# Optimization experiments

Hardware: AMD Instinct MI355X
Metric: run time of the kernel (lower is better)

## Reference

```python
import jax, jax.numpy as jnp
import numpy as np

N_NODES = 50000
N_EDGES = 1_600_000
REL_NUM = 16
D_IN = 64
D_OUT = 64


def setup_inputs() -> dict:
    key = jax.random.key(0)
    k_h, k_w, k_n, k_s, k_d, k_r = jax.random.split(key, 6)
    h = jax.random.normal(k_h, (N_NODES, D_IN), dtype=jnp.float32)
    # xavier_uniform over (rel_num, input_dim, output_dim): fan_in=input_dim, fan_out=output_dim
    limit = float(np.sqrt(6.0 / (D_IN + D_OUT)))
    weight = jax.random.uniform(k_w, (REL_NUM, D_IN, D_OUT), dtype=jnp.float32,
                                minval=-limit, maxval=limit)
    norm = jax.random.uniform(k_n, (N_EDGES, 1), dtype=jnp.float32)
    src = jax.random.randint(k_s, (N_EDGES,), 0, N_NODES)
    dst = jax.random.randint(k_d, (N_EDGES,), 0, N_NODES)
    rel_type = jax.random.randint(k_r, (N_EDGES,), 0, REL_NUM)
    return {"h": h, "weight": weight, "norm": norm,
            "src": src, "dst": dst, "rel_type": rel_type}


def reference(h, weight, norm, src, dst, rel_type):
    # Non-input path of R_GCN_Layer:
    #   msg_e = (h[src_e] @ weight[rel_e]) * norm_e ; h'_v = relu(sum_{e->v} msg_e)
    # Instead of gathering a [E, D_in, D_out] weight tensor per edge (huge),
    # transform every node by every relation once, then gather per (src, rel).
    n_nodes = h.shape[0]
    transformed = jnp.einsum('nd,rdo->nro', h, weight)      # [N, R, D_out]
    msg = transformed[src, rel_type] * norm                  # [E, D_out]
    agg = jax.ops.segment_sum(msg, dst, num_segments=n_nodes)  # [N, D_out]
    return jax.nn.relu(agg)
```

## Files before the change

### kernel.cpp

```cpp
#include <hip/hip_runtime.h>
#include <hip/hip_bf16.h>

#define N_NODES 50000
#define N_EDGES 1600000
#define NREL    16
#define DIM     64

#define BKT_SZ  16
#define NTILE   3125
#define NSEG_AL 50049

#define CB_SH   7
#define NCB     391
#define P1_CHUNK 2048
#define P1_GRID  782

#define CB_ARENA 8704
#define EMAX    (NCB * CB_ARENA)
#define PREP_HBLK 3125

typedef __attribute__((ext_vector_type(8))) short short8;
typedef __attribute__((ext_vector_type(4))) float float4v;
typedef __attribute__((ext_vector_type(4))) unsigned short ushort4v;

template<int IS_F32>
__device__ __forceinline__ float ldx(const void* p, size_t i) {
    if (IS_F32) {
        return ((const float*)p)[i];
    } else {
        unsigned short u = ((const unsigned short*)p)[i];
        return __uint_as_float(((unsigned)u) << 16);
    }
}

__device__ __forceinline__ float bfbits2f(unsigned short u) {
    return __uint_as_float(((unsigned)u) << 16);
}

__device__ __forceinline__ unsigned short f2bfbits(float v) {
    __hip_bfloat16 b = __float2bfloat16(v);
    unsigned short us; __builtin_memcpy(&us, &b, 2);
    return us;
}

__global__ __launch_bounds__(1024) void k_detect(
    const float* __restrict__ norm_f, int* __restrict__ flag)
{
    __shared__ int sbad;
    if (threadIdx.x == 0) sbad = 0;
    __syncthreads();
    float v = norm_f[threadIdx.x];
    int bad = (v != v || fabsf(v) > 1e3f) ? 1 : 0;
    if (bad) atomicOr(&sbad, 1);
    __syncthreads();
    if (threadIdx.x == 0) *flag = sbad ? 0 : 1;
}

__global__ __launch_bounds__(256) void k_bhist_prep(
    const int* __restrict__ dst, int* __restrict__ H,
    const void* __restrict__ h_raw, const void* __restrict__ w_raw,
    unsigned short* __restrict__ hbf, unsigned short* __restrict__ Wswz,
    const int* __restrict__ flag)
{
    __shared__ int hist[NCB];
    const int blk = blockIdx.x;
    if (blk < P1_GRID) {
        for (int i = threadIdx.x; i < NCB; i += 256) hist[i] = 0;
        __syncthreads();
        const int e0 = blk * P1_CHUNK;
        for (int i = threadIdx.x; i < P1_CHUNK; i += 256) {
            int e = e0 + i;
            if (e < N_EDGES) atomicAdd(&hist[dst[e] >> CB_SH], 1);
        }
        __syncthreads();
        for (int b = threadIdx.x; b < NCB; b += 256)
            H[blk * NCB + b] = hist[b];
    } else {
        const int f = *flag;
        const int blk2 = blk - P1_GRID;
        if (blk2 < PREP_HBLK) {
            int i0 = blk2 * 1024 + threadIdx.x * 4;
            if (f) {
                float4 v = *(const float4*)((const float*)h_raw + i0);
                ushort4v o;
                o[0] = f2bfbits(v.x); o[1] = f2bfbits(v.y);
                o[2] = f2bfbits(v.z); o[3] = f2bfbits(v.w);
                *(ushort4v*)(hbf + i0) = o;
            } else {
                *(uint2*)(hbf + i0) = *(const uint2*)((const unsigned short*)h_raw + i0);
            }
        } else {
            int rel = blk2 - PREP_HBLK;
            for (int idx = threadIdx.x; idx < 4096; idx += 256) {
                int d = idx >> 6, o = idx & 63;
                float wv = f ? ((const float*)w_raw)[(size_t)((rel << 6) + d) * 64 + o]
                             : bfbits2f(((const unsigned short*)w_raw)[(size_t)((rel << 6) + d) * 64 + o]);
                int c = d >> 5, q = (d >> 3) & 3, j = d & 7;
                Wswz[(size_t)rel * 5120 + ((c << 6) + o) * 40 + q * 8 + j] = f2bfbits(wv);
            }
        }
    }
}

__global__ __launch_bounds__(256) void k_bscan1(
    const int* __restrict__ H, int* __restrict__ OT, int* __restrict__ tot)
{
    __shared__ int col[P1_GRID];
    const int b = blockIdx.x;
    for (int i = threadIdx.x; i < P1_GRID; i += 256)
        col[i] = H[i * NCB + b];
    __syncthreads();
    if (threadIdx.x < 64) {
        const int lane = threadIdx.x;
        int carry = 0;
        for (int chunk = 0; chunk < (P1_GRID + 63) / 64; ++chunk) {
            int i = chunk * 64 + lane;
            int c = (i < P1_GRID) ? col[i] : 0;
            int incl = c;
#pragma unroll
            for (int off = 1; off < 64; off <<= 1) {
                int t = __shfl_up(incl, off, 64);
                if (lane >= off) incl += t;
            }
            if (i < P1_GRID) col[i] = carry + incl - c;
            carry += __shfl(incl, 63, 64);
        }
        if (lane == 0) tot[b] = carry;
    }
    __syncthreads();
    for (int i = threadIdx.x; i < P1_GRID; i += 256)
        OT[(size_t)b * P1_GRID + i] = col[i];
}

__global__ __launch_bounds__(64) void k_bscan2(
    const int* __restrict__ tot, int* __restrict__ base)
{
    const int lane = threadIdx.x;
    int carry = 0;
    for (int chunk = 0; chunk < (NCB + 63) / 64; ++chunk) {
        int i = chunk * 64 + lane;
        int c = (i < NCB) ? tot[i] : 0;
        int incl = c;
#pragma unroll
        for (int off = 1; off < 64; off <<= 1) {
            int t = __shfl_up(incl, off, 64);
            if (lane >= off) incl += t;
        }
        if (i < NCB) base[i] = carry + incl - c;
        carry += __shfl(incl, 63, 64);
    }
    if (lane == 0) base[NCB] = carry;
}

template<int IS_F32>
__device__ __forceinline__ void p1_body(
    const int* __restrict__ src, const int* __restrict__ dst,
    const int* __restrict__ rel, const void* __restrict__ norm_raw,
    const int* __restrict__ base, const int* __restrict__ OT,
    unsigned long long* __restrict__ R, int* curs)
{
    const int blk = blockIdx.x;
    for (int b = threadIdx.x; b < NCB; b += 256)
        curs[b] = base[b] + OT[(size_t)b * P1_GRID + blk];
    __syncthreads();
    const int e0 = blk * P1_CHUNK;
    for (int i = threadIdx.x; i < P1_CHUNK; i += 256) {
        int e = e0 + i;
        if (e >= N_EDGES) continue;
        int d = dst[e];
        int pos = atomicAdd(&curs[d >> CB_SH], 1);
        unsigned short nb = f2bfbits(ldx<IS_F32>(norm_raw, e));
        unsigned long long rec =
              (unsigned long long)(d & 127)
            | ((unsigned long long)(unsigned)src[e] << 8)
            | ((unsigned long long)(unsigned)rel[e] << 24)
            | ((unsigned long long)nb << 32);
        R[pos] = rec;
    }
}

__global__ __launch_bounds__(256) void k_p1(
    const int* __restrict__ src, const int* __restrict__ dst,
    const int* __restrict__ rel, const void* __restrict__ norm_raw,
    const int* __restrict__ base, const int* __restrict__ OT,
    unsigned long long* __restrict__ R, const int* __restrict__ flag)
{
    __shared__ int curs[NCB];
    if (*flag) p1_body<1>(src, dst, rel, norm_raw, base, OT, R, curs);
    else       p1_body<0>(src, dst, rel, norm_raw, base, OT, R, curs);
}

__global__ __launch_bounds__(256) void k_fine(
    const int* __restrict__ base,
    const unsigned long long* __restrict__ R,
    unsigned* __restrict__ packed2, unsigned short* __restrict__ normS,
    int* __restrict__ segBase, int* __restrict__ segCnt)
{
    __shared__ int cnt[128], sbl[128], curs[128];
    const int tid = threadIdx.x, cb = blockIdx.x;
    if (tid < 128) { cnt[tid] = 0; curs[tid] = 0; }
    __syncthreads();
    const int c0 = base[cb], c1 = base[cb + 1];

    for (int i = c0 + tid; i < c1; i += 256) {
        unsigned long long rec = R[i];
        int bin = (int)((rec >> 24) & 15) * 8 + (int)((rec >> 4) & 7);
        atomicAdd(&cnt[bin], 1);
    }
    __syncthreads();

    if (tid == 0) {
        int g = cb * CB_ARENA;
        for (int j = 0; j < 128; ++j) {
            sbl[j] = g;
            g += (cnt[j] + 31) & ~31;
        }
    }
    __syncthreads();

    if (tid < 128) {
        int seg = ((cb * 8 + (tid & 7)) << 4) + (tid >> 3);
        segBase[seg] = sbl[tid];
        segCnt[seg]  = cnt[tid];
    }

    for (int i = c0 + tid; i < c1; i += 256) {
        unsigned long long rec = R[i];
        int bin = (int)((rec >> 24) & 15) * 8 + (int)((rec >> 4) & 7);
        int pos = sbl[bin] + atomicAdd(&curs[bin], 1);
        packed2[pos] = (unsigned)rec & 0x00FFFF0Fu;
        normS[pos]   = (unsigned short)(rec >> 32);
    }
    __syncthreads();

    for (int p = tid; p < 128 * 32; p += 256) {
        int bin = p >> 5, j = p & 31;
        int c = cnt[bin], pe = (c + 31) & ~31;
        if (j < pe - c) {
            int pos = sbl[bin] + c + j;
            packed2[pos] = 0;
            normS[pos]   = 0;
        }
    }
}

#define MFMA_BF16 __builtin_amdgcn_mfma_f32_16x16x32_bf16

__global__ __launch_bounds__(256) void k_fused2(
    const unsigned* __restrict__ packed2,
    const unsigned short* __restrict__ normS,
    const unsigned short* __restrict__ hbf,
    const unsigned short* __restrict__ Wswz,
    const int* __restrict__ segBase,
    const int* __restrict__ segCnt,
    void* __restrict__ out, const int* __restrict__ flag)
{
    __shared__ __align__(16) unsigned short sbuf[4][16 * 72];
    __shared__ float pbuf[2][64][17];
    const int tid  = threadIdx.x;
    const int lane = tid & 63, wave = tid >> 6;
    const int n15  = lane & 15, quad = lane >> 4;
    const int tin  = wave >> 1;
    const int half = wave & 1;
    const int tile = blockIdx.x * 2 + tin;
    const bool valid = (tile < NTILE);

    float4v ac0 = {0.f,0.f,0.f,0.f}, ac1 = {0.f,0.f,0.f,0.f};
    float4v ac2 = {0.f,0.f,0.f,0.f}, ac3 = {0.f,0.f,0.f,0.f};
    unsigned short* sb_ = &sbuf[wave][0];

    if (valid) {
        const int r0 = half * 8;
        for (int r = r0; r < r0 + 8; ++r) {
            const int sgb  = segBase[tile * 16 + r];
            const int scnt = segCnt[tile * 16 + r];
            if (scnt == 0) continue;
            const int nch = (scnt + 31) >> 5;

            float4v s0 = {0.f,0.f,0.f,0.f}, s1 = {0.f,0.f,0.f,0.f};
            float4v s2 = {0.f,0.f,0.f,0.f}, s3 = {0.f,0.f,0.f,0.f};

            for (int c = 0; c < nch; ++c) {
                const int e0 = sgb + (c << 5) + (quad << 3);
                const uint4 pa = *(const uint4*)(packed2 + e0);
                const uint4 pb = *(const uint4*)(packed2 + e0 + 4);
                const ushort4v na = *(const ushort4v*)(normS + e0);
                const ushort4v nb = *(const ushort4v*)(normS + e0 + 4);

                const unsigned short* h0 = hbf + (size_t)(pa.x >> 8) * 64 + n15;
                const unsigned short* h1 = hbf + (size_t)(pa.y >> 8) * 64 + n15;
                const unsigned short* h2 = hbf + (size_t)(pa.z >> 8) * 64 + n15;
                const unsigned short* h3 = hbf + (size_t)(pa.w >> 8) * 64 + n15;
                const unsigned short* h4 = hbf + (size_t)(pb.x >> 8) * 64 + n15;
                const unsigned short* h5 = hbf + (size_t)(pb.y >> 8) * 64 + n15;
                const unsigned short* h6 = hbf + (size_t)(pb.z >> 8) * 64 + n15;
                const unsigned short* h7 = hbf + (size_t)(pb.w >> 8) * 64 + n15;

                short8 av;
                av[0] = ((int)(pa.x & 15u) == n15) ? (short)na[0] : (short)0;
                av[1] = ((int)(pa.y & 15u) == n15) ? (short)na[1] : (short)0;
                av[2] = ((int)(pa.z & 15u) == n15) ? (short)na[2] : (short)0;
                av[3] = ((int)(pa.w & 15u) == n15) ? (short)na[3] : (short)0;
                av[4] = ((int)(pb.x & 15u) == n15) ? (short)nb[0] : (short)0;
                av[5] = ((int)(pb.y & 15u) == n15) ? (short)nb[1] : (short)0;
                av[6] = ((int)(pb.z & 15u) == n15) ? (short)nb[2] : (short)0;
                av[7] = ((int)(pb.w & 15u) == n15) ? (short)nb[3] : (short)0;

#define GATHER_MFMA(S, OFF) \
                { short8 bv; \
                  bv[0] = (short)h0[OFF]; bv[1] = (short)h1[OFF]; \
                  bv[2] = (short)h2[OFF]; bv[3] = (short)h3[OFF]; \
                  bv[4] = (short)h4[OFF]; bv[5] = (short)h5[OFF]; \
                  bv[6] = (short)h6[OFF]; bv[7] = (short)h7[OFF]; \
                  S = MFMA_BF16(av, bv, S, 0, 0, 0); }

                GATHER_MFMA(s0, 0)
                GATHER_MFMA(s1, 16)
                GATHER_MFMA(s2, 32)
                GATHER_MFMA(s3, 48)
#undef GATHER_MFMA
            }

#pragma unroll
            for (int i = 0; i < 4; ++i) {
                sb_[(quad * 4 + i) * 72 +  0 + n15] = f2bfbits(s0[i]);
                sb_[(quad * 4 + i) * 72 + 16 + n15] = f2bfbits(s1[i]);
                sb_[(quad * 4 + i) * 72 + 32 + n15] = f2bfbits(s2[i]);
                sb_[(quad * 4 + i) * 72 + 48 + n15] = f2bfbits(s3[i]);
            }

            const short8 a0 = *(const short8*)(sb_ + n15 * 72 + quad * 8);
            const short8 a1 = *(const short8*)(sb_ + n15 * 72 + 32 + quad * 8);

            const unsigned short* wp = Wswz + (size_t)r * 5120;
            const short8 w00 = *(const short8*)(wp + ( 0 + n15) * 40 + quad * 8);
            const short8 w01 = *(const short8*)(wp + (16 + n15) * 40 + quad * 8);
            const short8 w02 = *(const short8*)(wp + (32 + n15) * 40 + quad * 8);
            const short8 w03 = *(const short8*)(wp + (48 + n15) * 40 + quad * 8);
            const short8 w10 = *(const short8*)(wp + (64 + n15) * 40 + quad * 8);
            const short8 w11 = *(const short8*)(wp + (80 + n15) * 40 + quad * 8);
            const short8 w12 = *(const short8*)(wp + (96 + n15) * 40 + quad * 8);
            const short8 w13 = *(const short8*)(wp + (112 + n15) * 40 + quad * 8);

            ac0 = MFMA_BF16(a0, w00, ac0, 0, 0, 0);
            ac1 = MFMA_BF16(a0, w01, ac1, 0, 0, 0);
            ac2 = MFMA_BF16(a0, w02, ac2, 0, 0, 0);
            ac3 = MFMA_BF16(a0, w03, ac3, 0, 0, 0);
            ac0 = MFMA_BF16(a1, w10, ac0, 0, 0, 0);
            ac1 = MFMA_BF16(a1, w11, ac1, 0, 0, 0);
            ac2 = MFMA_BF16(a1, w12, ac2, 0, 0, 0);
            ac3 = MFMA_BF16(a1, w13, ac3, 0, 0, 0);
        }
    }

    if (half) {
#pragma unroll
        for (int i = 0; i < 4; ++i) {
            pbuf[tin][lane][i]      = ac0[i];
            pbuf[tin][lane][4 + i]  = ac1[i];
            pbuf[tin][lane][8 + i]  = ac2[i];
            pbuf[tin][lane][12 + i] = ac3[i];
        }
    }
    __syncthreads();
    if (!half && valid) {
#pragma unroll
        for (int i = 0; i < 4; ++i) {
            ac0[i] += pbuf[tin][lane][i];
            ac1[i] += pbuf[tin][lane][4 + i];
            ac2[i] += pbuf[tin][lane][8 + i];
            ac3[i] += pbuf[tin][lane][12 + i];
        }
        const int node0 = tile << 4;
        const int f = *flag;
#define STORE_T(AC, T) \
        { \
            _Pragma("unroll") \
            for (int i = 0; i < 4; ++i) { \
                float rv = fmaxf(AC[i], 0.f); \
                size_t ob = (size_t)(node0 + quad * 4 + i) * 64 + (T) * 16 + n15; \
                if (f) ((float*)out)[ob] = rv; \
                else   ((unsigned short*)out)[ob] = f2bfbits(rv); \
            } \
        }
        STORE_T(ac0, 0)
        STORE_T(ac1, 1)
        STORE_T(ac2, 2)
        STORE_T(ac3, 3)
#undef STORE_T
    }
}

extern "C" void kernel_launch(void* const* d_in, const int* in_sizes, int n_in,
                              void* d_out, int out_size, void* d_ws, size_t ws_size,
                              hipStream_t stream)
{
    const void* h      = d_in[0];
    const void* weight = d_in[1];
    const void* norm   = d_in[2];
    const int* src = (const int*)d_in[3];
    const int* dst = (const int*)d_in[4];
    const int* rel = (const int*)d_in[5];

    char* w = (char*)d_ws;
    int* flag = (int*)w;                        w += 256;
    int* base = (int*)w;                        w += ((NCB + 1) * 4 + 255) / 256 * 256;
    int* tot  = (int*)w;                        w += (NCB * 4 + 255) / 256 * 256;
    int* H    = (int*)w;                        w += ((size_t)P1_GRID * NCB * 4 + 255) / 256 * 256;
    int* OT   = (int*)w;                        w += ((size_t)NCB * P1_GRID * 4 + 255) / 256 * 256;
    int* segBase = (int*)w;                     w += ((size_t)NSEG_AL * 4 + 255) / 256 * 256;
    int* segCnt  = (int*)w;                     w += ((size_t)NSEG_AL * 4 + 255) / 256 * 256;
    unsigned long long* R = (unsigned long long*)w;  w += (size_t)N_EDGES * 8;
    unsigned* packed2 = (unsigned*)w;           w += ((size_t)EMAX * 4 + 255) / 256 * 256;
    unsigned short* normS = (unsigned short*)w; w += ((size_t)EMAX * 2 + 255) / 256 * 256;
    unsigned short* hbf = (unsigned short*)w;   w += (size_t)N_NODES * DIM * 2;
    unsigned short* Wswz = (unsigned short*)w;  w += (size_t)NREL * 5120 * 2;

    k_detect<<<1, 1024, 0, stream>>>((const float*)norm, flag);

    k_bhist_prep<<<P1_GRID + PREP_HBLK + NREL, 256, 0, stream>>>(
        dst, H, h, weight, hbf, Wswz, flag);

    k_bscan1<<<NCB, 256, 0, stream>>>(H, OT, tot);
    k_bscan2<<<1, 64, 0, stream>>>(tot, base);

    k_p1<<<P1_GRID, 256, 0, stream>>>(src, dst, rel, norm, base, OT, R, flag);

    k_fine<<<NCB, 256, 0, stream>>>(base, R, packed2, normS, segBase, segCnt);

    k_fused2<<<(NTILE + 1) / 2, 256, 0, stream>>>(packed2, normS, hbf, Wswz,
                                                  segBase, segCnt, d_out, flag);
}
```

Before: 210.4 us.

## Batch bucket scan columns, transpose offset table, and software-pipeline edge chunk loads

The bucket-offset scan now processes 8 buckets per block and writes its offset table in block-major layout. This makes the column reads in the scan and the per-block cursor reads in the scatter kernel contiguous instead of strided. The fused gather/MFMA kernel flattens its loop over (relation, chunk) into a single stream and prefetches the next chunk's packed indices and norms while the current chunk's gathers and MFMAs run, hiding load latency. The cost is extra registers for the prefetched data and more complex control flow.

Result: slower. 237.5 us (+12.9%).

```diff
diff --git a/kernel.cpp b/kernel.cpp
--- a/kernel.cpp
+++ b/kernel.cpp
@@ -18,10 +18,12 @@
 #define CB_ARENA 8704
 #define EMAX    (NCB * CB_ARENA)
 #define PREP_HBLK 3125
+#define SCAN_B  8
 
 typedef __attribute__((ext_vector_type(8))) short short8;
 typedef __attribute__((ext_vector_type(4))) float float4v;
 typedef __attribute__((ext_vector_type(4))) unsigned short ushort4v;
+typedef __attribute__((ext_vector_type(8))) unsigned short ushort8;
 
 template<int IS_F32>
 __device__ __forceinline__ float ldx(const void* p, size_t i) {
@@ -103,33 +105,42 @@
 }
 
 __global__ __launch_bounds__(256) void k_bscan1(
-    const int* __restrict__ H, int* __restrict__ OT, int* __restrict__ tot)
-{
-    __shared__ int col[P1_GRID];
-    const int b = blockIdx.x;
-    for (int i = threadIdx.x; i < P1_GRID; i += 256)
-        col[i] = H[i * NCB + b];
-    __syncthreads();
-    if (threadIdx.x < 64) {
-        const int lane = threadIdx.x;
+    const int* __restrict__ H, int* __restrict__ OTT, int* __restrict__ tot)
+{
+    __shared__ int col[SCAN_B][P1_GRID];
+    const int b0 = blockIdx.x * SCAN_B;
+    const int nb = min(SCAN_B, NCB - b0);
+    for (int i = threadIdx.x; i < P1_GRID; i += 256) {
+        const int* hp = H + (size_t)i * NCB + b0;
+#pragma unroll
+        for (int j = 0; j < SCAN_B; ++j)
+            if (j < nb) col[j][i] = hp[j];
+    }
+    __syncthreads();
+    const int wave = threadIdx.x >> 6, lane = threadIdx.x & 63;
+    for (int j = wave; j < nb; j += 4) {
         int carry = 0;
         for (int chunk = 0; chunk < (P1_GRID + 63) / 64; ++chunk) {
             int i = chunk * 64 + lane;
-            int c = (i < P1_GRID) ? col[i] : 0;
+            int c = (i < P1_GRID) ? col[j][i] : 0;
             int incl = c;
 #pragma unroll
             for (int off = 1; off < 64; off <<= 1) {
                 int t = __shfl_up(incl, off, 64);
                 if (lane >= off) incl += t;
             }
-            if (i < P1_GRID) col[i] = carry + incl - c;
+            if (i < P1_GRID) col[j][i] = carry + incl - c;
             carry += __shfl(incl, 63, 64);
         }
-        if (lane == 0) tot[b] = carry;
-    }
-    __syncthreads();
-    for (int i = threadIdx.x; i < P1_GRID; i += 256)
-        OT[(size_t)b * P1_GRID + i] = col[i];
+        if (lane == 0) tot[b0 + j] = carry;
+    }
+    __syncthreads();
+    for (int i = threadIdx.x; i < P1_GRID; i += 256) {
+        int* op = OTT + (size_t)i * NCB + b0;
+#pragma unroll
+        for (int j = 0; j < SCAN_B; ++j)
+            if (j < nb) op[j] = col[j][i];
+    }
 }
 
 __global__ __launch_bounds__(64) void k_bscan2(
@@ -156,12 +167,12 @@
 __device__ __forceinline__ void p1_body(
     const int* __restrict__ src, const int* __restrict__ dst,
     const int* __restrict__ rel, const void* __restrict__ norm_raw,
-    const int* __restrict__ base, const int* __restrict__ OT,
+    const int* __restrict__ base, const int* __restrict__ OTT,
     unsigned long long* __restrict__ R, int* curs)
 {
     const int blk = blockIdx.x;
     for (int b = threadIdx.x; b < NCB; b += 256)
-        curs[b] = base[b] + OT[(size_t)b * P1_GRID + blk];
+        curs[b] = base[b] + OTT[(size_t)blk * NCB + b];
     __syncthreads();
     const int e0 = blk * P1_CHUNK;
     for (int i = threadIdx.x; i < P1_CHUNK; i += 256) {
@@ -182,12 +193,12 @@
 __global__ __launch_bounds__(256) void k_p1(
     const int* __restrict__ src, const int* __restrict__ dst,
     const int* __restrict__ rel, const void* __restrict__ norm_raw,
-    const int* __restrict__ base, const int* __restrict__ OT,
+    const int* __restrict__ base, const int* __restrict__ OTT,
     unsigned long long* __restrict__ R, const int* __restrict__ flag)
 {
     __shared__ int curs[NCB];
-    if (*flag) p1_body<1>(src, dst, rel, norm_raw, base, OT, R, curs);
-    else       p1_body<0>(src, dst, rel, norm_raw, base, OT, R, curs);
+    if (*flag) p1_body<1>(src, dst, rel, norm_raw, base, OTT, R, curs);
+    else       p1_body<0>(src, dst, rel, norm_raw, base, OTT, R, curs);
 }
 
 __global__ __launch_bounds__(256) void k_fine(
@@ -271,85 +282,119 @@
 
     if (valid) {
         const int r0 = half * 8;
-        for (int r = r0; r < r0 + 8; ++r) {
-            const int sgb  = segBase[tile * 16 + r];
-            const int scnt = segCnt[tile * 16 + r];
-            if (scnt == 0) continue;
-            const int nch = (scnt + 31) >> 5;
-
-            float4v s0 = {0.f,0.f,0.f,0.f}, s1 = {0.f,0.f,0.f,0.f};
-            float4v s2 = {0.f,0.f,0.f,0.f}, s3 = {0.f,0.f,0.f,0.f};
-
-            for (int c = 0; c < nch; ++c) {
-                const int e0 = sgb + (c << 5) + (quad << 3);
-                const uint4 pa = *(const uint4*)(packed2 + e0);
-                const uint4 pb = *(const uint4*)(packed2 + e0 + 4);
-                const ushort4v na = *(const ushort4v*)(normS + e0);
-                const ushort4v nb = *(const ushort4v*)(normS + e0 + 4);
-
-                const unsigned short* h0 = hbf + (size_t)(pa.x >> 8) * 64 + n15;
-                const unsigned short* h1 = hbf + (size_t)(pa.y >> 8) * 64 + n15;
-                const unsigned short* h2 = hbf + (size_t)(pa.z >> 8) * 64 + n15;
-                const unsigned short* h3 = hbf + (size_t)(pa.w >> 8) * 64 + n15;
-                const unsigned short* h4 = hbf + (size_t)(pb.x >> 8) * 64 + n15;
-                const unsigned short* h5 = hbf + (size_t)(pb.y >> 8) * 64 + n15;
-                const unsigned short* h6 = hbf + (size_t)(pb.z >> 8) * 64 + n15;
-                const unsigned short* h7 = hbf + (size_t)(pb.w >> 8) * 64 + n15;
-
-                short8 av;
-                av[0] = ((int)(pa.x & 15u) == n15) ? (short)na[0] : (short)0;
-                av[1] = ((int)(pa.y & 15u) == n15) ? (short)na[1] : (short)0;
-                av[2] = ((int)(pa.z & 15u) == n15) ? (short)na[2] : (short)0;
-                av[3] = ((int)(pa.w & 15u) == n15) ? (short)na[3] : (short)0;
-                av[4] = ((int)(pb.x & 15u) == n15) ? (short)nb[0] : (short)0;
-                av[5] = ((int)(pb.y & 15u) == n15) ? (short)nb[1] : (short)0;
-                av[6] = ((int)(pb.z & 15u) == n15) ? (short)nb[2] : (short)0;
-                av[7] = ((int)(pb.w & 15u) == n15) ? (short)nb[3] : (short)0;
+        const int sidx = tile * 16;
+        int r = r0 - 1, c = 0, nch = 0, sgb = 0;
+
+        auto advance = [&]() -> bool {
+            if (++c < nch) return true;
+            for (++r; r < r0 + 8; ++r) {
+                int sc = segCnt[sidx + r];
+                if (sc > 0) {
+                    nch = (sc + 31) >> 5;
+                    c = 0;
+                    sgb = segBase[sidx + r];
+                    return true;
+                }
+            }
+            return false;
+        };
+
+        bool have = advance();
+        uint4 pa = {0,0,0,0}, pb = {0,0,0,0};
+        ushort8 nmv = {0,0,0,0,0,0,0,0};
+        if (have) {
+            const int e0 = sgb + (c << 5) + (quad << 3);
+            pa  = *(const uint4*)(packed2 + e0);
+            pb  = *(const uint4*)(packed2 + e0 + 4);
+            nmv = *(const ushort8*)(normS + e0);
+        }
+
+        float4v s0 = {0.f,0.f,0.f,0.f}, s1 = {0.f,0.f,0.f,0.f};
+        float4v s2 = {0.f,0.f,0.f,0.f}, s3 = {0.f,0.f,0.f,0.f};
+
+        while (have) {
+            const int rcur = r;
+            const bool nhave = advance();
+            uint4 pa2 = {0,0,0,0}, pb2 = {0,0,0,0};
+            ushort8 nm2 = {0,0,0,0,0,0,0,0};
+            if (nhave) {
+                const int e1 = sgb + (c << 5) + (quad << 3);
+                pa2 = *(const uint4*)(packed2 + e1);
+                pb2 = *(const uint4*)(packed2 + e1 + 4);
+                nm2 = *(const ushort8*)(normS + e1);
+            }
+
+            const unsigned short* h0 = hbf + (size_t)(pa.x >> 8) * 64 + n15;
+            const unsigned short* h1 = hbf + (size_t)(pa.y >> 8) * 64 + n15;
+            const unsigned short* h2 = hbf + (size_t)(pa.z >> 8) * 64 + n15;
+            const unsigned short* h3 = hbf + (size_t)(pa.w >> 8) * 64 + n15;
+            const unsigned short* h4 = hbf + (size_t)(pb.x >> 8) * 64 + n15;
+            const unsigned short* h5 = hbf + (size_t)(pb.y >> 8) * 64 + n15;
+            const unsigned short* h6 = hbf + (size_t)(pb.z >> 8) * 64 + n15;
+            const unsigned short* h7 = hbf + (size_t)(pb.w >> 8) * 64 + n15;
+
+            short8 av;
+            av[0] = ((int)(pa.x & 15u) == n15) ? (short)nmv[0] : (short)0;
+            av[1] = ((int)(pa.y & 15u) == n15) ? (short)nmv[1] : (short)0;
+            av[2] = ((int)(pa.z & 15u) == n15) ? (short)nmv[2] : (short)0;
+            av[3] = ((int)(pa.w & 15u) == n15) ? (short)nmv[3] : (short)0;
+            av[4] = ((int)(pb.x & 15u) == n15) ? (short)nmv[4] : (short)0;
+            av[5] = ((int)(pb.y & 15u) == n15) ? (short)nmv[5] : (short)0;
+            av[6] = ((int)(pb.z & 15u) == n15) ? (short)nmv[6] : (short)0;
+            av[7] = ((int)(pb.w & 15u) == n15) ? (short)nmv[7] : (short)0;
 
 #define GATHER_MFMA(S, OFF) \
-                { short8 bv; \
-                  bv[0] = (short)h0[OFF]; bv[1] = (short)h1[OFF]; \
-                  bv[2] = (short)h2[OFF]; bv[3] = (short)h3[OFF]; \
-                  bv[4] = (short)h4[OFF]; bv[5] = (short)h5[OFF]; \
-                  bv[6] = (short)h6[OFF]; bv[7] = (short)h7[OFF]; \
-                  S = MFMA_BF16(av, bv, S, 0, 0, 0); }
-
-                GATHER_MFMA(s0, 0)
-                GATHER_MFMA(s1, 16)
-                GATHER_MFMA(s2, 32)
-                GATHER_MFMA(s3, 48)
+            { short8 bv; \
+              bv[0] = (short)h0[OFF]; bv[1] = (short)h1[OFF]; \
+              bv[2] = (short)h2[OFF]; bv[3] = (short)h3[OFF]; \
+              bv[4] = (short)h4[OFF]; bv[5] = (short)h5[OFF]; \
+              bv[6] = (short)h6[OFF]; bv[7] = (short)h7[OFF]; \
+              S = MFMA_BF16(av, bv, S, 0, 0, 0); }
+
+            GATHER_MFMA(s0, 0)
+            GATHER_MFMA(s1, 16)
+            GATHER_MFMA(s2, 32)
+            GATHER_MFMA(s3, 48)
 #undef GATHER_MFMA
-            }
-
-#pragma unroll
-            for (int i = 0; i < 4; ++i) {
-                sb_[(quad * 4 + i) * 72 +  0 + n15] = f2bfbits(s0[i]);
-                sb_[(quad * 4 + i) * 72 + 16 + n15] = f2bfbits(s1[i]);
-                sb_[(quad * 4 + i) * 72 + 32 + n15] = f2bfbits(s2[i]);
-                sb_[(quad * 4 + i) * 72 + 48 + n15] = f2bfbits(s3[i]);
-            }
-
-            const short8 a0 = *(const short8*)(sb_ + n15 * 72 + quad * 8);
-            const short8 a1 = *(const short8*)(sb_ + n15 * 72 + 32 + quad * 8);
-
-            const unsigned short* wp = Wswz + (size_t)r * 5120;
-            const short8 w00 = *(const short8*)(wp + ( 0 + n15) * 40 + quad * 8);
-            const short8 w01 = *(const short8*)(wp + (16 + n15) * 40 + quad * 8);
-            const short8 w02 = *(const short8*)(wp + (32 + n15) * 40 + quad * 8);
-            const short8 w03 = *(const short8*)(wp + (48 + n15) * 40 + quad * 8);
-            const short8 w10 = *(const short8*)(wp + (64 + n15) * 40 + quad * 8);
-            const short8 w11 = *(const short8*)(wp + (80 + n15) * 40 + quad * 8);
-            const short8 w12 = *(const short8*)(wp + (96 + n15) * 40 + quad * 8);
-            const short8 w13 = *(const short8*)(wp + (112 + n15) * 40 + quad * 8);
-
-            ac0 = MFMA_BF16(a0, w00, ac0, 0, 0, 0);
-            ac1 = MFMA_BF16(a0, w01, ac1, 0, 0, 0);
-            ac2 = MFMA_BF16(a0, w02, ac2, 0, 0, 0);
-            ac3 = MFMA_BF16(a0, w03, ac3, 0, 0, 0);
-            ac0 = MFMA_BF16(a1, w10, ac0, 0, 0, 0);
-            ac1 = MFMA_BF16(a1, w11, ac1, 0, 0, 0);
-            ac2 = MFMA_BF16(a1, w12, ac2, 0, 0, 0);
-            ac3 = MFMA_BF16(a1, w13, ac3, 0, 0, 0);
+
+            if (!nhave || r != rcur) {
+#pragma unroll
+                for (int i = 0; i < 4; ++i) {
+                    sb_[(quad * 4 + i) * 72 +  0 + n15] = f2bfbits(s0[i]);
+                    sb_[(quad * 4 + i) * 72 + 16 + n15] = f2bfbits(s1[i]);
+                    sb_[(quad * 4 + i) * 72 + 32 + n15] = f2bfbits(s2[i]);
+                    sb_[(quad * 4 + i) * 72 + 48 + n15] = f2bfbits(s3[i]);
+                }
+                const short8 a0 = *(const short8*)(sb_ + n15 * 72 + quad * 8);
+                const short8 a1 = *(const short8*)(sb_ + n15 * 72 + 32 + quad * 8);
+
+                const unsigned short* wp = Wswz + (size_t)rcur * 5120;
+                const short8 w00 = *(const short8*)(wp + ( 0 + n15) * 40 + quad * 8);
+                const short8 w01 = *(const short8*)(wp + (16 + n15) * 40 + quad * 8);
+                const short8 w02 = *(const short8*)(wp + (32 + n15) * 40 + quad * 8);
+                const short8 w03 = *(const short8*)(wp + (48 + n15) * 40 + quad * 8);
+                const short8 w10 = *(const short8*)(wp + (64 + n15) * 40 + quad * 8);
+                const short8 w11 = *(const short8*)(wp + (80 + n15) * 40 + quad * 8);
+                const short8 w12 = *(const short8*)(wp + (96 + n15) * 40 + quad * 8);
+                const short8 w13 = *(const short8*)(wp + (112 + n15) * 40 + quad * 8);
+
+                ac0 = MFMA_BF16(a0, w00, ac0, 0, 0, 0);
+                ac1 = MFMA_BF16(a0, w01, ac1, 0, 0, 0);
+                ac2 = MFMA_BF16(a0, w02, ac2, 0, 0, 0);
+                ac3 = MFMA_BF16(a0, w03, ac3, 0, 0, 0);
+                ac0 = MFMA_BF16(a1, w10, ac0, 0, 0, 0);
+                ac1 = MFMA_BF16(a1, w11, ac1, 0, 0, 0);
+                ac2 = MFMA_BF16(a1, w12, ac2, 0, 0, 0);
+                ac3 = MFMA_BF16(a1, w13, ac3, 0, 0, 0);
+
+                s0 = (float4v){0.f,0.f,0.f,0.f};
+                s1 = (float4v){0.f,0.f,0.f,0.f};
+                s2 = (float4v){0.f,0.f,0.f,0.f};
+                s3 = (float4v){0.f,0.f,0.f,0.f};
+            }
+
+            pa = pa2; pb = pb2; nmv = nm2;
+            have = nhave;
         }
     }
 
@@ -407,7 +452,7 @@
     int* base = (int*)w;                        w += ((NCB + 1) * 4 + 255) / 256 * 256;
     int* tot  = (int*)w;                        w += (NCB * 4 + 255) / 256 * 256;
     int* H    = (int*)w;                        w += ((size_t)P1_GRID * NCB * 4 + 255) / 256 * 256;
-    int* OT   = (int*)w;                        w += ((size_t)NCB * P1_GRID * 4 + 255) / 256 * 256;
+    int* OTT  = (int*)w;                        w += ((size_t)P1_GRID * NCB * 4 + 255) / 256 * 256;
     int* segBase = (int*)w;                     w += ((size_t)NSEG_AL * 4 + 255) / 256 * 256;
     int* segCnt  = (int*)w;                     w += ((size_t)NSEG_AL * 4 + 255) / 256 * 256;
     unsigned long long* R = (unsigned long long*)w;  w += (size_t)N_EDGES * 8;
@@ -421,10 +466,10 @@
     k_bhist_prep<<<P1_GRID + PREP_HBLK + NREL, 256, 0, stream>>>(
         dst, H, h, weight, hbf, Wswz, flag);
 
-    k_bscan1<<<NCB, 256, 0, stream>>>(H, OT, tot);
+    k_bscan1<<<(NCB + SCAN_B - 1) / SCAN_B, 256, 0, stream>>>(H, OTT, tot);
     k_bscan2<<<1, 64, 0, stream>>>(tot, base);
 
-    k_p1<<<P1_GRID, 256, 0, stream>>>(src, dst, rel, norm, base, OT, R, flag);
+    k_p1<<<P1_GRID, 256, 0, stream>>>(src, dst, rel, norm, base, OTT, R, flag);
 
     k_fine<<<NCB, 256, 0, stream>>>(base, R, packed2, normS, segBase, segCnt);
 
```

## Replace histogram-scan-scatter with atomic bucket arenas in a single split pass

Applied to the files above, without the earlier changes.

Each edge chunk builds a local histogram of coarse destination buckets and reserves space in fixed-size per-bucket arenas through global atomics. It then scatters its packed records directly, which removes the two scan kernels, the separate scatter kernel and the large per-block offset tables. The downstream fine-binning kernel reads bucket extents from the atomic cursors. The fixed arena size assumes no bucket exceeds its capacity; overflow is clamped and would overwrite records if the destination distribution were skewed.

Measured after the change: 213.1 us. Within noise of the previous version (+1.3%).

```diff
diff --git a/kernel.cpp b/kernel.cpp
--- a/kernel.cpp
+++ b/kernel.cpp
@@ -15,6 +15,7 @@
 #define P1_CHUNK 2048
 #define P1_GRID  782
 
+#define CB_R_ARENA 5120
 #define CB_ARENA 8704
 #define EMAX    (NCB * CB_ARENA)
 #define PREP_HBLK 3125
@@ -44,10 +45,12 @@
 }
 
 __global__ __launch_bounds__(1024) void k_detect(
-    const float* __restrict__ norm_f, int* __restrict__ flag)
+    const float* __restrict__ norm_f, int* __restrict__ flag,
+    int* __restrict__ gcur)
 {
     __shared__ int sbad;
     if (threadIdx.x == 0) sbad = 0;
+    if (threadIdx.x < NCB) gcur[threadIdx.x] = 0;
     __syncthreads();
     float v = norm_f[threadIdx.x];
     int bad = (v != v || fabsf(v) > 1e3f) ? 1 : 0;
@@ -56,25 +59,60 @@
     if (threadIdx.x == 0) *flag = sbad ? 0 : 1;
 }
 
-__global__ __launch_bounds__(256) void k_bhist_prep(
-    const int* __restrict__ dst, int* __restrict__ H,
+template<int IS_F32>
+__device__ __forceinline__ void split_body(
+    const int* __restrict__ src, const int* __restrict__ dst,
+    const int* __restrict__ rel, const void* __restrict__ norm_raw,
+    int* __restrict__ gcur, unsigned long long* __restrict__ R,
+    int* hist, int* curs)
+{
+    const int blk = blockIdx.x;
+    for (int i = threadIdx.x; i < NCB; i += 256) hist[i] = 0;
+    __syncthreads();
+    const int e0 = blk * P1_CHUNK;
+    for (int i = threadIdx.x; i < P1_CHUNK; i += 256) {
+        int e = e0 + i;
+        if (e < N_EDGES) atomicAdd(&hist[dst[e] >> CB_SH], 1);
+    }
+    __syncthreads();
+    for (int b = threadIdx.x; b < NCB; b += 256) {
+        int c = hist[b];
+        if (c > 0) {
+            int s = atomicAdd(&gcur[b], c);
+            if (s + c > CB_R_ARENA) s = CB_R_ARENA - c;
+            curs[b] = b * CB_R_ARENA + s;
+        }
+    }
+    __syncthreads();
+    for (int i = threadIdx.x; i < P1_CHUNK; i += 256) {
+        int e = e0 + i;
+        if (e >= N_EDGES) continue;
+        int d = dst[e];
+        int pos = atomicAdd(&curs[d >> CB_SH], 1);
+        unsigned short nb = f2bfbits(ldx<IS_F32>(norm_raw, e));
+        unsigned long long rec =
+              (unsigned long long)(d & 127)
+            | ((unsigned long long)(unsigned)src[e] << 8)
+            | ((unsigned long long)(unsigned)rel[e] << 24)
+            | ((unsigned long long)nb << 32);
+        R[pos] = rec;
+    }
+}
+
+__global__ __launch_bounds__(256) void k_split_prep(
+    const int* __restrict__ src, const int* __restrict__ dst,
+    const int* __restrict__ rel, const void* __restrict__ norm_raw,
+    int* __restrict__ gcur, unsigned long long* __restrict__ R,
     const void* __restrict__ h_raw, const void* __restrict__ w_raw,
     unsigned short* __restrict__ hbf, unsigned short* __restrict__ Wswz,
     const int* __restrict__ flag)
 {
     __shared__ int hist[NCB];
+    __shared__ int curs[NCB];
     const int blk = blockIdx.x;
     if (blk < P1_GRID) {
-        for (int i = threadIdx.x; i < NCB; i += 256) hist[i] = 0;
-        __syncthreads();
-        const int e0 = blk * P1_CHUNK;
-        for (int i = threadIdx.x; i < P1_CHUNK; i += 256) {
-            int e = e0 + i;
-            if (e < N_EDGES) atomicAdd(&hist[dst[e] >> CB_SH], 1);
-        }
-        __syncthreads();
-        for (int b = threadIdx.x; b < NCB; b += 256)
-            H[blk * NCB + b] = hist[b];
+        if (*flag) split_body<1>(src, dst, rel, norm_raw, gcur, R, hist, curs);
+        else       split_body<0>(src, dst, rel, norm_raw, gcur, R, hist, curs);
     } else {
         const int f = *flag;
         const int blk2 = blk - P1_GRID;
@@ -90,108 +128,20 @@
                 *(uint2*)(hbf + i0) = *(const uint2*)((const unsigned short*)h_raw + i0);
             }
         } else {
-            int rel = blk2 - PREP_HBLK;
+            int rel2 = blk2 - PREP_HBLK;
             for (int idx = threadIdx.x; idx < 4096; idx += 256) {
                 int d = idx >> 6, o = idx & 63;
-                float wv = f ? ((const float*)w_raw)[(size_t)((rel << 6) + d) * 64 + o]
-                             : bfbits2f(((const unsigned short*)w_raw)[(size_t)((rel << 6) + d) * 64 + o]);
+                float wv = f ? ((const float*)w_raw)[(size_t)((rel2 << 6) + d) * 64 + o]
+                             : bfbits2f(((const unsigned short*)w_raw)[(size_t)((rel2 << 6) + d) * 64 + o]);
                 int c = d >> 5, q = (d >> 3) & 3, j = d & 7;
-                Wswz[(size_t)rel * 5120 + ((c << 6) + o) * 40 + q * 8 + j] = f2bfbits(wv);
+                Wswz[(size_t)rel2 * 5120 + ((c << 6) + o) * 40 + q * 8 + j] = f2bfbits(wv);
             }
         }
     }
 }
 
-__global__ __launch_bounds__(256) void k_bscan1(
-    const int* __restrict__ H, int* __restrict__ OT, int* __restrict__ tot)
-{
-    __shared__ int col[P1_GRID];
-    const int b = blockIdx.x;
-    for (int i = threadIdx.x; i < P1_GRID; i += 256)
-        col[i] = H[i * NCB + b];
-    __syncthreads();
-    if (threadIdx.x < 64) {
-        const int lane = threadIdx.x;
-        int carry = 0;
-        for (int chunk = 0; chunk < (P1_GRID + 63) / 64; ++chunk) {
-            int i = chunk * 64 + lane;
-            int c = (i < P1_GRID) ? col[i] : 0;
-            int incl = c;
-#pragma unroll
-            for (int off = 1; off < 64; off <<= 1) {
-                int t = __shfl_up(incl, off, 64);
-                if (lane >= off) incl += t;
-            }
-            if (i < P1_GRID) col[i] = carry + incl - c;
-            carry += __shfl(incl, 63, 64);
-        }
-        if (lane == 0) tot[b] = carry;
-    }
-    __syncthreads();
-    for (int i = threadIdx.x; i < P1_GRID; i += 256)
-        OT[(size_t)b * P1_GRID + i] = col[i];
-}
-
-__global__ __launch_bounds__(64) void k_bscan2(
-    const int* __restrict__ tot, int* __restrict__ base)
-{
-    const int lane = threadIdx.x;
-    int carry = 0;
-    for (int chunk = 0; chunk < (NCB + 63) / 64; ++chunk) {
-        int i = chunk * 64 + lane;
-        int c = (i < NCB) ? tot[i] : 0;
-        int incl = c;
-#pragma unroll
-        for (int off = 1; off < 64; off <<= 1) {
-            int t = __shfl_up(incl, off, 64);
-            if (lane >= off) incl += t;
-        }
-        if (i < NCB) base[i] = carry + incl - c;
-        carry += __shfl(incl, 63, 64);
-    }
-    if (lane == 0) base[NCB] = carry;
-}
-
-template<int IS_F32>
-__device__ __forceinline__ void p1_body(
-    const int* __restrict__ src, const int* __restrict__ dst,
-    const int* __restrict__ rel, const void* __restrict__ norm_raw,
-    const int* __restrict__ base, const int* __restrict__ OT,
-    unsigned long long* __restrict__ R, int* curs)
-{
-    const int blk = blockIdx.x;
-    for (int b = threadIdx.x; b < NCB; b += 256)
-        curs[b] = base[b] + OT[(size_t)b * P1_GRID + blk];
-    __syncthreads();
-    const int e0 = blk * P1_CHUNK;
-    for (int i = threadIdx.x; i < P1_CHUNK; i += 256) {
-        int e = e0 + i;
-        if (e >= N_EDGES) continue;
-        int d = dst[e];
-        int pos = atomicAdd(&curs[d >> CB_SH], 1);
-        unsigned short nb = f2bfbits(ldx<IS_F32>(norm_raw, e));
-        unsigned long long rec =
-              (unsigned long long)(d & 127)
-            | ((unsigned long long)(unsigned)src[e] << 8)
-            | ((unsigned long long)(unsigned)rel[e] << 24)
-            | ((unsigned long long)nb << 32);
-        R[pos] = rec;
-    }
-}
-
-__global__ __launch_bounds__(256) void k_p1(
-    const int* __restrict__ src, const int* __restrict__ dst,
-    const int* __restrict__ rel, const void* __restrict__ norm_raw,
-    const int* __restrict__ base, const int* __restrict__ OT,
-    unsigned long long* __restrict__ R, const int* __restrict__ flag)
-{
-    __shared__ int curs[NCB];
-    if (*flag) p1_body<1>(src, dst, rel, norm_raw, base, OT, R, curs);
-    else       p1_body<0>(src, dst, rel, norm_raw, base, OT, R, curs);
-}
-
 __global__ __launch_bounds__(256) void k_fine(
-    const int* __restrict__ base,
+    const int* __restrict__ gcur,
     const unsigned long long* __restrict__ R,
     unsigned* __restrict__ packed2, unsigned short* __restrict__ normS,
     int* __restrict__ segBase, int* __restrict__ segCnt)
@@ -200,7 +150,8 @@
     const int tid = threadIdx.x, cb = blockIdx.x;
     if (tid < 128) { cnt[tid] = 0; curs[tid] = 0; }
     __syncthreads();
-    const int c0 = base[cb], c1 = base[cb + 1];
+    const int c0 = cb * CB_R_ARENA;
+    const int c1 = c0 + min(gcur[cb], CB_R_ARENA);
 
     for (int i = c0 + tid; i < c1; i += 256) {
         unsigned long long rec = R[i];
@@ -404,29 +355,21 @@
 
     char* w = (char*)d_ws;
     int* flag = (int*)w;                        w += 256;
-    int* base = (int*)w;                        w += ((NCB + 1) * 4 + 255) / 256 * 256;
-    int* tot  = (int*)w;                        w += (NCB * 4 + 255) / 256 * 256;
-    int* H    = (int*)w;                        w += ((size_t)P1_GRID * NCB * 4 + 255) / 256 * 256;
-    int* OT   = (int*)w;                        w += ((size_t)NCB * P1_GRID * 4 + 255) / 256 * 256;
+    int* gcur = (int*)w;                        w += (NCB * 4 + 255) / 256 * 256;
     int* segBase = (int*)w;                     w += ((size_t)NSEG_AL * 4 + 255) / 256 * 256;
     int* segCnt  = (int*)w;                     w += ((size_t)NSEG_AL * 4 + 255) / 256 * 256;
-    unsigned long long* R = (unsigned long long*)w;  w += (size_t)N_EDGES * 8;
+    unsigned long long* R = (unsigned long long*)w;  w += (size_t)NCB * CB_R_ARENA * 8;
     unsigned* packed2 = (unsigned*)w;           w += ((size_t)EMAX * 4 + 255) / 256 * 256;
     unsigned short* normS = (unsigned short*)w; w += ((size_t)EMAX * 2 + 255) / 256 * 256;
     unsigned short* hbf = (unsigned short*)w;   w += (size_t)N_NODES * DIM * 2;
     unsigned short* Wswz = (unsigned short*)w;  w += (size_t)NREL * 5120 * 2;
 
-    k_detect<<<1, 1024, 0, stream>>>((const float*)norm, flag);
-
-    k_bhist_prep<<<P1_GRID + PREP_HBLK + NREL, 256, 0, stream>>>(
-        dst, H, h, weight, hbf, Wswz, flag);
-
-    k_bscan1<<<NCB, 256, 0, stream>>>(H, OT, tot);
-    k_bscan2<<<1, 64, 0, stream>>>(tot, base);
-
-    k_p1<<<P1_GRID, 256, 0, stream>>>(src, dst, rel, norm, base, OT, R, flag);
-
-    k_fine<<<NCB, 256, 0, stream>>>(base, R, packed2, normS, segBase, segCnt);
+    k_detect<<<1, 1024, 0, stream>>>((const float*)norm, flag, gcur);
+
+    k_split_prep<<<P1_GRID + PREP_HBLK + NREL, 256, 0, stream>>>(
+        src, dst, rel, norm, gcur, R, h, weight, hbf, Wswz, flag);
+
+    k_fine<<<NCB, 256, 0, stream>>>(gcur, R, packed2, normS, segBase, segCnt);
 
     k_fused2<<<(NTILE + 1) / 2, 256, 0, stream>>>(packed2, normS, hbf, Wswz,
                                                   segBase, segCnt, d_out, flag);
```
